# Kernel tuning notes

Hardware: AMD Instinct MI355X
Metric: run time of the kernel (lower is better)

## Reference

```python
import jax, jax.numpy as jnp
import numpy as np

DIM = 768
NUM_HEADS = 16
D = DIM // NUM_HEADS  # 48


def setup_inputs() -> dict:
    key = jax.random.key(0)
    ks = jax.random.split(key, 7)
    x = jax.random.normal(ks[0], (4, 4096, DIM), dtype=jnp.float32)
    # Linear weights stored as [in, out] for x @ W + b
    s = 1.0 / np.sqrt(DIM)
    Wq = jax.random.uniform(ks[1], (DIM, D), jnp.float32, -s, s)
    Wk = jax.random.uniform(ks[2], (DIM, D), jnp.float32, -s, s)
    Wv = jax.random.uniform(ks[3], (DIM, D), jnp.float32, -s, s)
    bq = jax.random.uniform(ks[4], (D,), jnp.float32, -s, s)
    bk = jax.random.uniform(ks[5], (D,), jnp.float32, -s, s)
    bv = jax.random.uniform(ks[6], (D,), jnp.float32, -s, s)
    return {"x": x, "Wq": Wq, "bq": bq, "Wk": Wk, "bk": bk, "Wv": Wv, "bv": bv}


def reference(x, Wq, bq, Wk, bk, Wv, bv):
    # q, k, v: [B, S, D]
    q = x @ Wq + bq
    k = x @ Wk + bk
    v = x @ Wv + bv
    scale = 1.0 / jnp.sqrt(jnp.asarray(D, dtype=q.dtype))
    # scores: [B, S_q, S_k]
    scores = jnp.einsum("bqd,bkd->bqk", q, k) * scale
    # NOTE: softmax over dim=1 = the QUERY axis (faithful to original torch code)
    qk = jax.nn.softmax(scores, axis=1)
    # dropout is identity in eval mode (deterministic reference)
    attn = jnp.einsum("bqk,bkd->bqd", qk, v)
    return attn
```

## Files before the change

kernel.cpp:

```cpp
#include <hip/hip_runtime.h>
#include <hip/hip_bf16.h>

#define NB 4
#define SEQ 4096
#define CDIM 768
#define HD 48

typedef __attribute__((ext_vector_type(8))) __bf16 bf16x8;
typedef __attribute__((ext_vector_type(16))) float f32x16;

static constexpr float SCALE_LOG2E = 0.20823542135164923f;

__device__ __forceinline__ bf16x8 ldg8(const __hip_bfloat16* p) {
    uint4 u = *reinterpret_cast<const uint4*>(p);
    bf16x8 r;
    __builtin_memcpy(&r, &u, 16);
    return r;
}
__device__ __forceinline__ unsigned pk2(float lo, float hi) {
    const __hip_bfloat16 a = __float2bfloat16(lo);
    const __hip_bfloat16 b = __float2bfloat16(hi);
    unsigned short ua, ub;
    __builtin_memcpy(&ua, &a, 2);
    __builtin_memcpy(&ub, &b, 2);
    return (unsigned)ua | ((unsigned)ub << 16);
}
__device__ __forceinline__ bf16x8 mk8(unsigned w0, unsigned w1, unsigned w2, unsigned w3) {
    const uint4 u = make_uint4(w0, w1, w2, w3);
    bf16x8 r;
    __builtin_memcpy(&r, &u, 16);
    return r;
}
__device__ __forceinline__ size_t fragOff(int tile, int s, int h) {
    return (((size_t)tile * 3 + s) * 2 + h) * 256;
}

__global__ __launch_bounds__(256) void prep_kernel(
    const float* __restrict__ Wq, const float* __restrict__ Wk,
    const float* __restrict__ Wv,
    const float* __restrict__ bq, const float* __restrict__ bk,
    const float* __restrict__ bv,
    __hip_bfloat16* __restrict__ Wf, float* __restrict__ bias)
{
    const int g = blockIdx.x * 256 + threadIdx.x;
    if (g < 15360) {
        const int rem  = g % 3072;
        const int nt   = g / 3072;
        const int ks   = rem >> 6;
        const int l2   = rem & 63;
        const int hh   = l2 >> 5;
        const int lane = l2 & 31;
        const int n    = nt * 32 + lane;
        const float* src = (n < 48) ? Wq : (n < 96) ? Wk : (n < 144) ? Wv : nullptr;
        const int col = (n < 48) ? n : (n < 96) ? (n - 48) : (n - 96);
        #pragma unroll
        for (int j = 0; j < 8; ++j) {
            const int k = ks * 16 + hh * 8 + j;
            const float wv = src ? src[(size_t)k * HD + col] : 0.0f;
            Wf[(size_t)g * 8 + j] = __float2bfloat16(wv);
        }
    }
    if (blockIdx.x == 0 && threadIdx.x < 160) {
        const int t = threadIdx.x;
        bias[t] = (t < 48) ? bq[t] : (t < 96) ? bk[t - 48] : (t < 144) ? bv[t - 96] : 0.0f;
    }
}

__global__ __launch_bounds__(320) void proj_kernel(
    const float* __restrict__ x,
    const __hip_bfloat16* __restrict__ Wf, const float* __restrict__ bias,
    __hip_bfloat16* __restrict__ Qf, __hip_bfloat16* __restrict__ Kf,
    float* __restrict__ Vf)
{
    __shared__ __hip_bfloat16 xs[48 * 512];

    const int t   = threadIdx.x;
    const int w   = t >> 6;
    const int l   = t & 63;
    const int lo5 = l & 31, h = l >> 5;
    const int mt  = blockIdx.x;
    const int m0  = mt * 32;

    const float* xb = x + (size_t)m0 * CDIM;
    #pragma unroll
    for (int i = 0; i < 20; ++i) {
        const int c = i * 320 + t;
        if (c < 6144) {
            const int r   = c / 192;
            const int pos = c % 192;
            const int k   = pos * 4;
            const float4 v = *reinterpret_cast<const float4*>(xb + (size_t)r * CDIM + k);
            const int ks = k >> 4, hh = (k >> 3) & 1, j = k & 7;
            const uint2 d = make_uint2(pk2(v.x, v.y), pk2(v.z, v.w));
            *reinterpret_cast<uint2*>(&xs[ks * 512 + (hh * 32 + r) * 8 + j]) = d;
        }
    }
    __syncthreads();

    const __hip_bfloat16* bp = Wf + (size_t)w * 24576 + l * 8;
    f32x16 acc = {};
    #pragma unroll 8
    for (int ks = 0; ks < 48; ++ks) {
        bf16x8 a;
        __builtin_memcpy(&a, &xs[ks * 512 + l * 8], 16);
        const bf16x8 b = ldg8(bp + (size_t)ks * 512);
        acc = __builtin_amdgcn_mfma_f32_32x32x16_bf16(a, b, acc, 0, 0, 0);
    }

    const int n_g = w * 32 + lo5;
    const float bs = bias[n_g];
    if (n_g < 96) {
        const bool isQ = (n_g < 48);
        const int d  = isQ ? n_g : n_g - 48;
        const int s  = d >> 4;
        const int hf = (d >> 3) & 1;
        __hip_bfloat16* base = (isQ ? Qf : Kf) + fragOff(mt, s, hf) + (d & 7);
        #pragma unroll
        for (int r = 0; r < 16; ++r) {
            const int mrow = (r & 3) + 8 * (r >> 2) + 4 * h;
            float val = acc[r] + bs;
            if (isQ) val *= SCALE_LOG2E;
            base[mrow * 8] = __float2bfloat16(val);
        }
    } else if (n_g < 144) {
        const int d = n_g - 96;
        #pragma unroll
        for (int r = 0; r < 16; ++r) {
            const int m = m0 + (r & 3) + 8 * (r >> 2) + 4 * h;
            Vf[(size_t)m * HD + d] = acc[r] + bs;
        }
    }
}

__global__ __launch_bounds__(512) void stats_kernel(
    const __hip_bfloat16* __restrict__ Qf, const __hip_bfloat16* __restrict__ Kf,
    const float* __restrict__ Vf, __hip_bfloat16* __restrict__ Vt)
{
    __shared__ float part[8][32];
    __shared__ float linv[32];

    const int t   = threadIdx.x;
    const int w   = t >> 6;
    const int l   = t & 63;
    const int lo5 = l & 31, h = l >> 5;
    const int b       = blockIdx.y;
    const int ktile_l = blockIdx.x;
    const int ktile   = b * 128 + ktile_l;

    bf16x8 ka[3];
    #pragma unroll
    for (int s = 0; s < 3; ++s)
        ka[s] = ldg8(Kf + fragOff(ktile, s, h) + lo5 * 8);

    float lsum[16];
    #pragma unroll
    for (int r = 0; r < 16; ++r) lsum[r] = 0.0f;

    const int qt0 = b * 128 + w * 16;
    #pragma unroll 2
    for (int qq = 0; qq < 16; ++qq) {
        bf16x8 qb[3];
        #pragma unroll
        for (int s = 0; s < 3; ++s)
            qb[s] = ldg8(Qf + fragOff(qt0 + qq, s, h) + lo5 * 8);
        f32x16 acc = {};
        #pragma unroll
        for (int s = 0; s < 3; ++s)
            acc = __builtin_amdgcn_mfma_f32_32x32x16_bf16(ka[s], qb[s], acc, 0, 0, 0);
        #pragma unroll
        for (int r = 0; r < 16; ++r) lsum[r] += __builtin_amdgcn_exp2f(acc[r]);
    }

    #pragma unroll
    for (int r = 0; r < 16; ++r) {
        lsum[r] += __shfl_xor(lsum[r], 1);
        lsum[r] += __shfl_xor(lsum[r], 2);
        lsum[r] += __shfl_xor(lsum[r], 4);
        lsum[r] += __shfl_xor(lsum[r], 8);
        lsum[r] += __shfl_xor(lsum[r], 16);
    }
    if (lo5 == 0) {
        #pragma unroll
        for (int r = 0; r < 16; ++r)
            part[w][(r & 3) + 8 * (r >> 2) + 4 * h] = lsum[r];
    }
    __syncthreads();
    if (t < 32) {
        float s = 0.0f;
        #pragma unroll
        for (int p = 0; p < 8; ++p) s += part[p][t];
        linv[t] = 1.0f / s;
    }
    __syncthreads();

    const int kp = t & 15;
    const int dg = t >> 4;
    const float f0 = linv[2 * kp], f1 = linv[2 * kp + 1];
    __hip_bfloat16* vtb = Vt + (size_t)ktile * 2048;
    const float* vfb = Vf + ((size_t)b * SEQ + ktile_l * 32 + 2 * kp) * HD;
    {
        const int d = dg;
        const float v0 = vfb[d], v1 = vfb[HD + d];
        *reinterpret_cast<unsigned*>(&vtb[d * 32 + 2 * kp]) = pk2(v0 * f0, v1 * f1);
    }
    if (dg < 16) {
        const int d = dg + 32;
        const float v0 = vfb[d], v1 = vfb[HD + d];
        *reinterpret_cast<unsigned*>(&vtb[d * 32 + 2 * kp]) = pk2(v0 * f0, v1 * f1);
    }
}

__global__ __launch_bounds__(512) void pv_kernel(
    const __hip_bfloat16* __restrict__ Qf, const __hip_bfloat16* __restrict__ Kf,
    const __hip_bfloat16* __restrict__ Vt, float* __restrict__ out)
{
    __shared__ float red[7][32][64];

    const int t   = threadIdx.x;
    const int w   = t >> 6;
    const int l   = t & 63;
    const int lo5 = l & 31, h = l >> 5;
    const int b       = blockIdx.y;
    const int qtile_l = blockIdx.x;
    const int qtile   = b * 128 + qtile_l;
    const int q0      = qtile_l * 32;
    const bool islo   = (h == 0);

    bf16x8 qb[3];
    #pragma unroll
    for (int s = 0; s < 3; ++s)
        qb[s] = ldg8(Qf + fragOff(qtile, s, h) + lo5 * 8);

    f32x16 o0 = {}, o1 = {};
    const int kt0 = b * 128 + w * 16;

    #pragma unroll 2
    for (int kk = 0; kk < 16; ++kk) {
        const int ktg = kt0 + kk;
        bf16x8 ka[3];
        #pragma unroll
        for (int s = 0; s < 3; ++s)
            ka[s] = ldg8(Kf + fragOff(ktg, s, h) + lo5 * 8);
        f32x16 acc = {};
        #pragma unroll
        for (int s = 0; s < 3; ++s)
            acc = __builtin_amdgcn_mfma_f32_32x32x16_bf16(ka[s], qb[s], acc, 0, 0, 0);

        float p[16];
        #pragma unroll
        for (int r = 0; r < 16; ++r) p[r] = __builtin_amdgcn_exp2f(acc[r]);

        const unsigned x0 = pk2(p[0],  p[1]),  x1 = pk2(p[2],  p[3]);
        const unsigned y0 = pk2(p[4],  p[5]),  y1 = pk2(p[6],  p[7]);
        const unsigned x2 = pk2(p[8],  p[9]),  x3 = pk2(p[10], p[11]);
        const unsigned y2 = pk2(p[12], p[13]), y3 = pk2(p[14], p[15]);

        unsigned w0, w1, w2, w3, w4, w5, w6, w7;
        { const unsigned ax = __shfl_xor(x0, 32), bx = __shfl_xor(y0, 32);
          w0 = islo ? x0 : bx;  w2 = islo ? ax : y0; }
        { const unsigned ax = __shfl_xor(x1, 32), bx = __shfl_xor(y1, 32);
          w1 = islo ? x1 : bx;  w3 = islo ? ax : y1; }
        { const unsigned ax = __shfl_xor(x2, 32), bx = __shfl_xor(y2, 32);
          w4 = islo ? x2 : bx;  w6 = islo ? ax : y2; }
        { const unsigned ax = __shfl_xor(x3, 32), bx = __shfl_xor(y3, 32);
          w5 = islo ? x3 : bx;  w7 = islo ? ax : y3; }

        const bf16x8 pa0 = mk8(w0, w1, w2, w3);
        const bf16x8 pa1 = mk8(w4, w5, w6, w7);

        const __hip_bfloat16* vt = Vt + (size_t)ktg * 2048 + lo5 * 32 + 8 * h;
        const bf16x8 va  = ldg8(vt);
        const bf16x8 vb2 = ldg8(vt + 16);
        const bf16x8 vc  = ldg8(vt + 1024);
        const bf16x8 vd  = ldg8(vt + 1024 + 16);
        o0 = __builtin_amdgcn_mfma_f32_32x32x16_bf16(pa0, va,  o0, 0, 0, 0);
        o0 = __builtin_amdgcn_mfma_f32_32x32x16_bf16(pa1, vb2, o0, 0, 0, 0);
        o1 = __builtin_amdgcn_mfma_f32_32x32x16_bf16(pa0, vc,  o1, 0, 0, 0);
        o1 = __builtin_amdgcn_mfma_f32_32x32x16_bf16(pa1, vd,  o1, 0, 0, 0);
    }

    if (w > 0) {
        #pragma unroll
        for (int r = 0; r < 16; ++r) {
            red[w - 1][r][l]      = o0[r];
            red[w - 1][16 + r][l] = o1[r];
        }
    }
    __syncthreads();
    if (w == 0) {
        #pragma unroll
        for (int r = 0; r < 16; ++r) {
            #pragma unroll
            for (int p = 0; p < 7; ++p) {
                o0[r] += red[p][r][l];
                o1[r] += red[p][16 + r][l];
            }
        }
        #pragma unroll
        for (int r = 0; r < 16; ++r) {
            const int q = q0 + (r & 3) + 8 * (r >> 2) + 4 * h;
            out[((size_t)(b * SEQ) + q) * HD + lo5] = o0[r];
            if (lo5 < 16)
                out[((size_t)(b * SEQ) + q) * HD + 32 + lo5] = o1[r];
        }
    }
}

extern "C" void kernel_launch(void* const* d_in, const int* in_sizes, int n_in,
                              void* d_out, int out_size, void* d_ws, size_t ws_size,
                              hipStream_t stream)
{
    const float* x  = (const float*)d_in[0];
    const float* Wq = (const float*)d_in[1];
    const float* bq = (const float*)d_in[2];
    const float* Wk = (const float*)d_in[3];
    const float* bk = (const float*)d_in[4];
    const float* Wv = (const float*)d_in[5];
    const float* bv = (const float*)d_in[6];
    float* out = (float*)d_out;

    const size_t FRAG = (size_t)512 * 6 * 256;
    __hip_bfloat16* Qf  = (__hip_bfloat16*)d_ws;
    __hip_bfloat16* Kf  = Qf + FRAG;
    float*          Vf  = (float*)(Kf + FRAG);
    __hip_bfloat16* Vt  = (__hip_bfloat16*)(Vf + (size_t)NB * SEQ * HD);
    __hip_bfloat16* Wf  = Vt + (size_t)NB * 128 * 2048;
    float*          bias = (float*)(Wf + (size_t)5 * 48 * 512);

    prep_kernel<<<dim3(60), 256, 0, stream>>>(Wq, Wk, Wv, bq, bk, bv, Wf, bias);
    proj_kernel<<<dim3(512), 320, 0, stream>>>(x, Wf, bias, Qf, Kf, Vf);
    stats_kernel<<<dim3(128, NB), 512, 0, stream>>>(Qf, Kf, Vf, Vt);
    pv_kernel<<<dim3(128, NB), 512, 0, stream>>>(Qf, Kf, Vt, out);
}
```

Baseline: 67.84 us.

## Use permlane32 swap, MFMA priority hints, and all-wave parallel output reduction

Each P-fragment exchange in the PV loop now uses v_permlane32_swap instead of a pair of cross-half shuffles plus selects, which cuts the instruction count of the inner loop. s_setprio(1) now wraps the MFMA sequences in the projection, column-sum and PV kernels, so waves issuing matrix ops get scheduling priority over waves doing loads and exp. The PV epilogue changes too: every wave writes its partial accumulators to shared memory, and all 512 threads sum the 8 partials and store them as float4. Before, wave 0 did the whole serial reduction and made scalar stores. This uses slightly more shared memory. The priority hints may help or hurt depending on occupancy.

```diff
diff --git a/kernel.cpp b/kernel.cpp
--- a/kernel.cpp
+++ b/kernel.cpp
@@ -30,6 +30,9 @@
     bf16x8 r;
     __builtin_memcpy(&r, &u, 16);
     return r;
+}
+__device__ __forceinline__ void plswap(unsigned& a, unsigned& b) {
+    asm volatile("v_permlane32_swap_b32 %0, %1" : "+v"(a), "+v"(b));
 }
 __device__ __forceinline__ size_t fragOff(int tile, int s, int h) {
     return (((size_t)tile * 3 + s) * 2 + h) * 256;
@@ -104,7 +107,9 @@
         bf16x8 a;
         __builtin_memcpy(&a, &xs[ks * 512 + l * 8], 16);
         const bf16x8 b = ldg8(bp + (size_t)ks * 512);
+        __builtin_amdgcn_s_setprio(1);
         acc = __builtin_amdgcn_mfma_f32_32x32x16_bf16(a, b, acc, 0, 0, 0);
+        __builtin_amdgcn_s_setprio(0);
     }
 
     const int n_g = w * 32 + lo5;
@@ -164,9 +169,11 @@
         for (int s = 0; s < 3; ++s)
             qb[s] = ldg8(Qf + fragOff(qt0 + qq, s, h) + lo5 * 8);
         f32x16 acc = {};
+        __builtin_amdgcn_s_setprio(1);
         #pragma unroll
         for (int s = 0; s < 3; ++s)
             acc = __builtin_amdgcn_mfma_f32_32x32x16_bf16(ka[s], qb[s], acc, 0, 0, 0);
+        __builtin_amdgcn_s_setprio(0);
         #pragma unroll
         for (int r = 0; r < 16; ++r) lsum[r] += __builtin_amdgcn_exp2f(acc[r]);
     }
@@ -214,7 +221,7 @@
     const __hip_bfloat16* __restrict__ Qf, const __hip_bfloat16* __restrict__ Kf,
     const __hip_bfloat16* __restrict__ Vt, float* __restrict__ out)
 {
-    __shared__ float red[7][32][64];
+    __shared__ float red[8][32][64];
 
     const int t   = threadIdx.x;
     const int w   = t >> 6;
@@ -224,7 +231,6 @@
     const int qtile_l = blockIdx.x;
     const int qtile   = b * 128 + qtile_l;
     const int q0      = qtile_l * 32;
-    const bool islo   = (h == 0);
 
     bf16x8 qb[3];
     #pragma unroll
@@ -242,28 +248,24 @@
         for (int s = 0; s < 3; ++s)
             ka[s] = ldg8(Kf + fragOff(ktg, s, h) + lo5 * 8);
         f32x16 acc = {};
+        __builtin_amdgcn_s_setprio(1);
         #pragma unroll
         for (int s = 0; s < 3; ++s)
             acc = __builtin_amdgcn_mfma_f32_32x32x16_bf16(ka[s], qb[s], acc, 0, 0, 0);
+        __builtin_amdgcn_s_setprio(0);
 
         float p[16];
         #pragma unroll
         for (int r = 0; r < 16; ++r) p[r] = __builtin_amdgcn_exp2f(acc[r]);
 
-        const unsigned x0 = pk2(p[0],  p[1]),  x1 = pk2(p[2],  p[3]);
-        const unsigned y0 = pk2(p[4],  p[5]),  y1 = pk2(p[6],  p[7]);
-        const unsigned x2 = pk2(p[8],  p[9]),  x3 = pk2(p[10], p[11]);
-        const unsigned y2 = pk2(p[12], p[13]), y3 = pk2(p[14], p[15]);
-
-        unsigned w0, w1, w2, w3, w4, w5, w6, w7;
-        { const unsigned ax = __shfl_xor(x0, 32), bx = __shfl_xor(y0, 32);
-          w0 = islo ? x0 : bx;  w2 = islo ? ax : y0; }
-        { const unsigned ax = __shfl_xor(x1, 32), bx = __shfl_xor(y1, 32);
-          w1 = islo ? x1 : bx;  w3 = islo ? ax : y1; }
-        { const unsigned ax = __shfl_xor(x2, 32), bx = __shfl_xor(y2, 32);
-          w4 = islo ? x2 : bx;  w6 = islo ? ax : y2; }
-        { const unsigned ax = __shfl_xor(x3, 32), bx = __shfl_xor(y3, 32);
-          w5 = islo ? x3 : bx;  w7 = islo ? ax : y3; }
+        unsigned w0 = pk2(p[0],  p[1]),  w1 = pk2(p[2],  p[3]);
+        unsigned w2 = pk2(p[4],  p[5]),  w3 = pk2(p[6],  p[7]);
+        unsigned w4 = pk2(p[8],  p[9]),  w5 = pk2(p[10], p[11]);
+        unsigned w6 = pk2(p[12], p[13]), w7 = pk2(p[14], p[15]);
+        plswap(w0, w2);
+        plswap(w1, w3);
+        plswap(w4, w6);
+        plswap(w5, w7);
 
         const bf16x8 pa0 = mk8(w0, w1, w2, w3);
         const bf16x8 pa1 = mk8(w4, w5, w6, w7);
@@ -273,35 +275,38 @@
         const bf16x8 vb2 = ldg8(vt + 16);
         const bf16x8 vc  = ldg8(vt + 1024);
         const bf16x8 vd  = ldg8(vt + 1024 + 16);
+        __builtin_amdgcn_s_setprio(1);
         o0 = __builtin_amdgcn_mfma_f32_32x32x16_bf16(pa0, va,  o0, 0, 0, 0);
         o0 = __builtin_amdgcn_mfma_f32_32x32x16_bf16(pa1, vb2, o0, 0, 0, 0);
         o1 = __builtin_amdgcn_mfma_f32_32x32x16_bf16(pa0, vc,  o1, 0, 0, 0);
         o1 = __builtin_amdgcn_mfma_f32_32x32x16_bf16(pa1, vd,  o1, 0, 0, 0);
-    }
-
-    if (w > 0) {
-        #pragma unroll
-        for (int r = 0; r < 16; ++r) {
-            red[w - 1][r][l]      = o0[r];
-            red[w - 1][16 + r][l] = o1[r];
-        }
+        __builtin_amdgcn_s_setprio(0);
+    }
+
+    #pragma unroll
+    for (int r = 0; r < 16; ++r) {
+        red[w][r][l]      = o0[r];
+        red[w][16 + r][l] = o1[r];
     }
     __syncthreads();
-    if (w == 0) {
-        #pragma unroll
-        for (int r = 0; r < 16; ++r) {
-            #pragma unroll
-            for (int p = 0; p < 7; ++p) {
-                o0[r] += red[p][r][l];
-                o1[r] += red[p][16 + r][l];
-            }
-        }
-        #pragma unroll
-        for (int r = 0; r < 16; ++r) {
-            const int q = q0 + (r & 3) + 8 * (r >> 2) + 4 * h;
-            out[((size_t)(b * SEQ) + q) * HD + lo5] = o0[r];
-            if (lo5 < 16)
-                out[((size_t)(b * SEQ) + q) * HD + 32 + lo5] = o1[r];
+
+    {
+        const int rr = t >> 4;
+        const int l0 = (t & 15) * 4;
+        float4 s = make_float4(0.f, 0.f, 0.f, 0.f);
+        #pragma unroll
+        for (int p = 0; p < 8; ++p) {
+            const float4 v = *reinterpret_cast<const float4*>(&red[p][rr][l0]);
+            s.x += v.x; s.y += v.y; s.z += v.z; s.w += v.w;
+        }
+        const int r   = rr & 15;
+        const int row = (r & 3) + 8 * (r >> 2) + 4 * (l0 >> 5);
+        if (rr < 16) {
+            *reinterpret_cast<float4*>(
+                &out[((size_t)(b * SEQ) + q0 + row) * HD + (l0 & 31)]) = s;
+        } else if ((l0 & 31) < 16) {
+            *reinterpret_cast<float4*>(
+                &out[((size_t)(b * SEQ) + q0 + row) * HD + 32 + (l0 & 31)]) = s;
         }
     }
 }
```

Result: no change. 68.35 us (+0.7%).
